# Kernel tuning notes

Measured on AMD Instinct MI355X. Metric: run time of the kernel, lower is better.

## Reference

```python
import jax, jax.numpy as jnp
import numpy as np

B, L, D, H, PD = 1, 512, 1024, 16, 128
HW = D // H  # 64


def _layernorm(x, g, b, eps=1e-5):
    mu = jnp.mean(x, axis=-1, keepdims=True)
    var = jnp.var(x, axis=-1, keepdims=True)
    return (x - mu) * jax.lax.rsqrt(var + eps) * g + b


def setup_inputs() -> dict:
    key = jax.random.key(0)
    ks = jax.random.split(key, 16)
    s = 0.02
    return {
        "sequence_state": jax.random.normal(ks[0], (B, L, D), jnp.float32),
        "pairwise_state": jax.random.normal(ks[1], (B, L, L, PD), jnp.float32),
        "mask": jnp.ones((B, L), dtype=bool),
        # layernorm before attention
        "ln1_g": jnp.ones((D,), jnp.float32),
        "ln1_b": jnp.zeros((D,), jnp.float32),
        # attention params (weights stored [in, out])
        "proj_w": jax.random.normal(ks[2], (D, 3 * H * HW), jnp.float32) * s,
        "g_w": jax.random.normal(ks[3], (D, H * HW), jnp.float32) * s,
        "g_b": jnp.ones((H * HW,), jnp.float32),
        "o_w": jax.random.normal(ks[4], (H * HW, D), jnp.float32) * s,
        "o_b": jnp.zeros((D,), jnp.float32),
        # pair-to-sequence bias
        "p2s_ln_g": jnp.ones((PD,), jnp.float32),
        "p2s_ln_b": jnp.zeros((PD,), jnp.float32),
        "p2s_w": jax.random.normal(ks[5], (PD, H), jnp.float32) * s,
        # residue MLP
        "mlp_ln_g": jnp.ones((D,), jnp.float32),
        "mlp_ln_b": jnp.zeros((D,), jnp.float32),
        "mlp_w1": jax.random.normal(ks[6], (D, 4 * D), jnp.float32) * s,
        "mlp_b1": jnp.zeros((4 * D,), jnp.float32),
        "mlp_w2": jax.random.normal(ks[7], (4 * D, D), jnp.float32) * s,
        "mlp_b2": jnp.zeros((D,), jnp.float32),
    }


def reference(sequence_state, pairwise_state, mask,
              ln1_g, ln1_b, proj_w, g_w, g_b, o_w, o_b,
              p2s_ln_g, p2s_ln_b, p2s_w,
              mlp_ln_g, mlp_ln_b, mlp_w1, mlp_b1, mlp_w2, mlp_b2):
    # PairToSequence: LN over pairwise feature dim, then project to per-head bias
    z = _layernorm(pairwise_state, p2s_ln_g, p2s_ln_b)
    bias = jnp.einsum("bqkp,ph->bhqk", z, p2s_w)  # [B,H,L,L]

    # Pre-attention layernorm
    y = _layernorm(sequence_state, ln1_g, ln1_b)

    # Gated attention with pairwise bias
    t = (y @ proj_w).reshape(B, L, H, 3 * HW)
    q, k, v = jnp.split(t, 3, axis=-1)  # each [B,L,H,HW]
    q = q * (HW ** -0.5)
    a = jnp.einsum("bqhc,bkhc->bhqk", q, k) + bias
    a = jnp.where(mask[:, None, None, :], a, -jnp.inf)
    a = jax.nn.softmax(a, axis=-1)
    o = jnp.einsum("bhqk,bkhc->bqhc", a, v).reshape(B, L, H * HW)
    gate = jax.nn.sigmoid(y @ g_w + g_b)
    o = (gate * o) @ o_w + o_b

    # residual (dropout=0 -> identity)
    s = sequence_state + o

    # ResidueMLP: x + Linear(ReLU(Linear(LN(x))))
    h = _layernorm(s, mlp_ln_g, mlp_ln_b)
    h = jax.nn.relu(h @ mlp_w1 + mlp_b1) @ mlp_w2 + mlp_b2
    return s + h
```

## Files before the change

### kernel.cpp

```cpp
#include <hip/hip_runtime.h>


typedef __attribute__((ext_vector_type(8))) short bfrag;
typedef __attribute__((ext_vector_type(4))) float f32x4;
typedef unsigned short ushort_t;
typedef unsigned int u32;

#define AS1 __attribute__((address_space(1)))
#define AS3 __attribute__((address_space(3)))

__device__ __forceinline__ void gll16(const void* g, void* l) {
  __builtin_amdgcn_global_load_lds((const AS1 u32*)g, (AS3 u32*)l, 16, 0, 0);
}

__device__ __forceinline__ unsigned short f2b(float x) {
  union { float f; unsigned u; } a; a.f = x;
  unsigned r = a.u + 0x7fffu + ((a.u >> 16) & 1u);
  return (unsigned short)(r >> 16);
}
__device__ __forceinline__ unsigned pack2(float a, float b) {
  return (unsigned)f2b(a) | ((unsigned)f2b(b) << 16);
}
__device__ __forceinline__ float b2f(ushort_t u) {
  union { float f; unsigned v; } a; a.v = ((unsigned)u) << 16; return a.f;
}

#define OFF_BIASH ((size_t)0)
#define OFF_Y     ((size_t)8388608)
#define OFF_QS    (OFF_Y    + (size_t)1048576)
#define OFF_KS    (OFF_QS   + (size_t)1048576)
#define OFF_VT    (OFF_KS   + (size_t)1048576)
#define OFF_GATE  (OFF_VT   + (size_t)1048576)
#define OFF_OG    (OFF_GATE + (size_t)2097152)
#define OFF_S     (OFF_OG   + (size_t)1048576)
#define OFF_HLN   (OFF_S    + (size_t)2097152)
#define OFF_H1    (OFF_HLN  + (size_t)1048576)
#define OFF_WPG   (OFF_H1   + (size_t)4194304)
#define OFF_WO    (OFF_WPG  + (size_t)8388608)
#define OFF_W1    (OFF_WO   + (size_t)2097152)
#define OFF_W2    (OFF_W1   + (size_t)8388608)

__device__ __forceinline__ void transp_tile(
    const float* __restrict__ W, ushort_t* __restrict__ Wt, int K, int N,
    int bx, int by, int tid, float* smem) {
  float (*tile)[65] = (float(*)[65])smem;
  int n0 = bx * 64, k0 = by * 64;
  int tr = tid >> 4, tc = (tid & 15) * 4;
#pragma unroll
  for (int i = 0; i < 4; i++) {
    int r = tr + i * 16;
    float4 v = *(const float4*)&W[(long)(k0 + r) * N + n0 + tc];
    tile[r][tc] = v.x; tile[r][tc + 1] = v.y; tile[r][tc + 2] = v.z; tile[r][tc + 3] = v.w;
  }
  __syncthreads();
  int nr = tid >> 2, kk = (tid & 3) * 16;
  ushort_t* dst = Wt + (long)(n0 + nr) * K + k0 + kk;
  uint4 q;
  q.x = pack2(tile[kk + 0][nr], tile[kk + 1][nr]);
  q.y = pack2(tile[kk + 2][nr], tile[kk + 3][nr]);
  q.z = pack2(tile[kk + 4][nr], tile[kk + 5][nr]);
  q.w = pack2(tile[kk + 6][nr], tile[kk + 7][nr]);
  *(uint4*)dst = q;
  uint4 q2;
  q2.x = pack2(tile[kk + 8][nr],  tile[kk + 9][nr]);
  q2.y = pack2(tile[kk + 10][nr], tile[kk + 11][nr]);
  q2.z = pack2(tile[kk + 12][nr], tile[kk + 13][nr]);
  q2.w = pack2(tile[kk + 14][nr], tile[kk + 15][nr]);
  *(uint4*)(dst + 8) = q2;
}

__global__ __launch_bounds__(256) void mega1(
    const float* __restrict__ pw,
    const float* __restrict__ p2s_g, const float* __restrict__ p2s_b,
    const float* __restrict__ p2s_w,
    const float* __restrict__ proj_w, const float* __restrict__ g_w,
    const float* __restrict__ o_w, const float* __restrict__ w1,
    const float* __restrict__ w2,
    const float* __restrict__ seq, const float* __restrict__ ln1_g,
    const float* __restrict__ ln1_b, const float* __restrict__ o_b,
    ushort_t* __restrict__ biasH, ushort_t* __restrict__ wpg,
    ushort_t* __restrict__ wo, ushort_t* __restrict__ w1t,
    ushort_t* __restrict__ w2t, ushort_t* __restrict__ ybf,
    float* __restrict__ sbuf) {
  __shared__ float smemF[5920];
  const int id = blockIdx.x, t = threadIdx.x;

  if (id < 4096) {
    ushort_t* wb  = (ushort_t*)smemF;
    ushort_t* zsb = wb + 2048;
    ushort_t* res = zsb + 64 * 136;
    const int w = t >> 6, lane = t & 63, ln = lane & 15, quad = lane >> 4;
    const long pair0 = (long)id * 64;
    const int p = t >> 2, j = t & 3;

#pragma unroll
    for (int i = t; i < 2048; i += 256) {
      int f = i >> 4, hh = i & 15;
      int chunk = f >> 5, q2 = (f >> 3) & 3, jj = f & 7;
      wb[(chunk * 64 + q2 * 16 + hh) * 8 + jj] = f2b(p2s_w[i]);
    }

    const float4* xsrc = (const float4*)(pw + (pair0 + p) * 128 + j * 32);
    float4 xv[8];
#pragma unroll
    for (int q = 0; q < 8; q++) xv[q] = xsrc[q];
    float s = 0.f, sq = 0.f;
#pragma unroll
    for (int q = 0; q < 8; q++) {
      s  += xv[q].x + xv[q].y + xv[q].z + xv[q].w;
      sq += xv[q].x*xv[q].x + xv[q].y*xv[q].y + xv[q].z*xv[q].z + xv[q].w*xv[q].w;
    }
    s  += __shfl_xor(s, 1);  s  += __shfl_xor(s, 2);
    sq += __shfl_xor(sq, 1); sq += __shfl_xor(sq, 2);
    float mu = s * (1.f / 128.f);
    float rs = rsqrtf(sq * (1.f / 128.f) - mu * mu + 1e-5f);

    const float4* g4 = (const float4*)(p2s_g + j * 32);
    const float4* b4 = (const float4*)(p2s_b + j * 32);
    uint4* zdst = (uint4*)&zsb[p * 136 + j * 32];
#pragma unroll
    for (int q = 0; q < 4; q++) {
      float4 x0 = xv[2*q], x1 = xv[2*q+1];
      float4 g0 = g4[2*q], g1 = g4[2*q+1];
      float4 b0 = b4[2*q], b1 = b4[2*q+1];
      uint4 o;
      o.x = pack2((x0.x-mu)*rs*g0.x + b0.x, (x0.y-mu)*rs*g0.y + b0.y);
      o.y = pack2((x0.z-mu)*rs*g0.z + b0.z, (x0.w-mu)*rs*g0.w + b0.w);
      o.z = pack2((x1.x-mu)*rs*g1.x + b1.x, (x1.y-mu)*rs*g1.y + b1.y);
      o.w = pack2((x1.z-mu)*rs*g1.z + b1.z, (x1.w-mu)*rs*g1.w + b1.w);
      zdst[q] = o;
    }
    __syncthreads();

    f32x4 acc = (f32x4){0.f, 0.f, 0.f, 0.f};
#pragma unroll
    for (int chunk = 0; chunk < 4; chunk++) {
      bfrag a  = *(const bfrag*)&zsb[(w * 16 + ln) * 136 + chunk * 32 + quad * 8];
      bfrag bf = *(const bfrag*)&wb[(chunk * 64 + quad * 16 + ln) * 8];
      acc = __builtin_amdgcn_mfma_f32_16x16x32_bf16(a, bf, acc, 0, 0, 0);
    }
    *(uint2*)&res[ln * 68 + w * 16 + quad * 4] =
        (uint2){pack2(acc[0], acc[1]), pack2(acc[2], acc[3])};
    __syncthreads();
    {
      int hh = t >> 4, base = (t & 15) * 4;
      *(uint2*)&biasH[(long)hh * 262144 + pair0 + base] =
          *(const uint2*)&res[hh * 68 + base];
    }
  } else if (id < 7424) {
    int j = id - 4096;
    if (j < 768)       transp_tile(proj_w, wpg, 1024, 3072, j % 48, j / 48, t, smemF);
    else if (j < 1024) { j -= 768;  transp_tile(g_w, wpg + (long)3072 * 1024, 1024, 1024, j % 16, j / 16, t, smemF); }
    else if (j < 1280) { j -= 1024; transp_tile(o_w, wo, 1024, 1024, j % 16, j / 16, t, smemF); }
    else if (j < 2304) { j -= 1280; transp_tile(w1, w1t, 1024, 4096, j % 64, j / 64, t, smemF); }
    else               { j -= 2304; transp_tile(w2, w2t, 4096, 1024, j % 16, j / 16, t, smemF); }
  } else {
    int row = id - 7424;
    long base = (long)row * 1024 + t * 4;
    float4 v = *(const float4*)(seq + base);
    float4 ob = *(const float4*)(o_b + t * 4);
    float4 sv; sv.x = v.x + ob.x; sv.y = v.y + ob.y; sv.z = v.z + ob.z; sv.w = v.w + ob.w;
    *(float4*)(sbuf + base) = sv;
    float s  = v.x + v.y + v.z + v.w;
    float sq = v.x*v.x + v.y*v.y + v.z*v.z + v.w*v.w;
#pragma unroll
    for (int k = 1; k < 64; k <<= 1) { s += __shfl_xor(s, k); sq += __shfl_xor(sq, k); }
    if ((t & 63) == 0) { smemF[t >> 6] = s; smemF[4 + (t >> 6)] = sq; }
    __syncthreads();
    s  = smemF[0] + smemF[1] + smemF[2] + smemF[3];
    sq = smemF[4] + smemF[5] + smemF[6] + smemF[7];
    float mu = s * (1.f / 1024.f);
    float rsd = rsqrtf(sq * (1.f / 1024.f) - mu * mu + 1e-5f);
    float4 gv = *(const float4*)(ln1_g + t * 4);
    float4 bv = *(const float4*)(ln1_b + t * 4);
    uint2 o;
    o.x = pack2((v.x - mu) * rsd * gv.x + bv.x, (v.y - mu) * rsd * gv.y + bv.y);
    o.y = pack2((v.z - mu) * rsd * gv.z + bv.z, (v.w - mu) * rsd * gv.w + bv.w);
    *(uint2*)(ybf + base) = o;
  }
}

template <int EPI>
__global__ __launch_bounds__(256) void gemm128(
    const ushort_t* __restrict__ A, const ushort_t* __restrict__ Bt,
    int lda, int ldb, int Ksplit,
    const float* __restrict__ bias1,
    float* __restrict__ outF, ushort_t* __restrict__ outH, int ldc,
    ushort_t* __restrict__ qs, ushort_t* __restrict__ ks,
    ushort_t* __restrict__ vt, float* __restrict__ gatebuf) {
  __shared__ ushort_t As[64 * 32];
  __shared__ ushort_t Bs[128 * 32];
  const int tid = threadIdx.x;
  const int w = tid >> 6, lane = tid & 63;
  const int ln = lane & 15, quad = lane >> 4;
  const int wm = w >> 1, wn = w & 1;
  const int m0 = blockIdx.y * 64, n0 = blockIdx.x * 128;
  const int z = blockIdx.z;
  const int Koff = (EPI == 7) ? z * Ksplit : 0;

  const ushort_t* ga  = A  + (long)(m0 + (tid >> 2)) * lda + Koff + (tid & 3) * 8;
  const ushort_t* gb0 = Bt + (long)(n0 + (tid >> 2)) * ldb + Koff + (tid & 3) * 8;
  const ushort_t* gb1 = gb0 + (long)64 * ldb;
  unsigned wofs = __builtin_amdgcn_readfirstlane(w * 1024);
  char* lA  = (char*)As + wofs;
  char* lB0 = (char*)Bs + wofs;
  char* lB1 = (char*)Bs + 4096 + wofs;

  f32x4 acc[2][4];
#pragma unroll
  for (int i = 0; i < 2; i++)
#pragma unroll
    for (int j = 0; j < 4; j++) acc[i][j] = (f32x4){0.f, 0.f, 0.f, 0.f};

  for (int k0 = 0; k0 < Ksplit; k0 += 32) {
    gll16(ga + k0, lA);
    gll16(gb0 + k0, lB0);
    gll16(gb1 + k0, lB1);
    __syncthreads();
    bfrag a0 = *(const bfrag*)&As[(wm * 32 + ln) * 32 + quad * 8];
    bfrag a1 = *(const bfrag*)&As[(wm * 32 + 16 + ln) * 32 + quad * 8];
#pragma unroll
    for (int bn = 0; bn < 4; bn++) {
      bfrag b = *(const bfrag*)&Bs[(wn * 64 + bn * 16 + ln) * 32 + quad * 8];
      acc[0][bn] = __builtin_amdgcn_mfma_f32_16x16x32_bf16(a0, b, acc[0][bn], 0, 0, 0);
      acc[1][bn] = __builtin_amdgcn_mfma_f32_16x16x32_bf16(a1, b, acc[1][bn], 0, 0, 0);
    }
    __syncthreads();
  }

#pragma unroll
  for (int am = 0; am < 2; am++) {
#pragma unroll
    for (int bn = 0; bn < 4; bn++) {
      int ocol = n0 + wn * 64 + bn * 16 + ln;
#pragma unroll
      for (int r = 0; r < 4; r++) {
        int orow = m0 + wm * 32 + am * 16 + quad * 4 + r;
        float v = acc[am][bn][r];
        if (EPI == 3) {
          v = fmaxf(v + bias1[ocol], 0.f);
          outH[(long)orow * ldc + ocol] = f2b(v);
        } else if (EPI == 6) {
          if (ocol < 3072) {
            int h = ocol / 192, j = ocol - h * 192;
            if (j < 64)       qs[((long)h * 512 + orow) * 64 + j] = f2b(v * 0.125f);
            else if (j < 128) ks[((long)h * 512 + orow) * 64 + (j - 64)] = f2b(v);
            else              vt[((long)h * 64 + (j - 128)) * 512 + orow] = f2b(v);
          } else {
            int gcol = ocol - 3072;
            float gv = v + bias1[gcol];
            gatebuf[(long)orow * 1024 + gcol] = 1.f / (1.f + __expf(-gv));
          }
        } else {
          atomicAdd(&outF[(long)orow * ldc + ocol], v);
        }
      }
    }
  }
}

__global__ __launch_bounds__(256) void flash_attn(
    const ushort_t* __restrict__ qs, const ushort_t* __restrict__ ks,
    const ushort_t* __restrict__ vt, const ushort_t* __restrict__ biasH,
    const float* __restrict__ gate, ushort_t* __restrict__ og) {
  __shared__ ushort_t Qs[32 * 72];
  __shared__ ushort_t Ks[64 * 72];
  __shared__ ushort_t Vs[64 * 72];
  __shared__ ushort_t Ps[32 * 72];
  __shared__ float redm[4][16];
  __shared__ float reds[4][16];
  const int tid = threadIdx.x;
  const int w = tid >> 6, lane = tid & 63, ln = lane & 15, quad = lane >> 4;
  const int wm = w >> 1, wn = w & 1;
  const int h = blockIdx.x, q0 = blockIdx.y * 32;

  {
    int r = tid >> 3, c0 = (tid & 7) * 8;
    *(uint4*)&Qs[r * 72 + c0] = *(const uint4*)(qs + ((long)(h * 512 + q0 + r)) * 64 + c0);
  }

  float m_[4], l_[4];
  f32x4 Oacc[2];
#pragma unroll
  for (int i = 0; i < 4; i++) { m_[i] = -1e30f; l_[i] = 0.f; }
  Oacc[0] = (f32x4){0.f,0.f,0.f,0.f};
  Oacc[1] = (f32x4){0.f,0.f,0.f,0.f};

  const int rkv = tid >> 2, ckv = (tid & 3) * 16;

  for (int kt = 0; kt < 8; kt++) {
    const int k0 = kt * 64;
    __syncthreads();
    { const ushort_t* srcK = ks + ((long)(h * 512 + k0 + rkv)) * 64 + ckv;
      *(uint4*)&Ks[rkv * 72 + ckv]     = *(const uint4*)srcK;
      *(uint4*)&Ks[rkv * 72 + ckv + 8] = *(const uint4*)(srcK + 8);
      const ushort_t* srcV = vt + ((long)(h * 64 + rkv)) * 512 + k0 + ckv;
      *(uint4*)&Vs[rkv * 72 + ckv]     = *(const uint4*)srcV;
      *(uint4*)&Vs[rkv * 72 + ckv + 8] = *(const uint4*)(srcV + 8); }

    f32x4 acc[2];
    const ushort_t* bp = biasH + ((long)h * 512 + q0 + wm * 16 + quad * 4) * 512
                         + k0 + wn * 32 + ln;
#pragma unroll
    for (int t4 = 0; t4 < 2; t4++)
#pragma unroll
      for (int rr = 0; rr < 4; rr++)
        acc[t4][rr] = b2f(bp[(long)rr * 512 + t4 * 16]);

    __syncthreads();
#pragma unroll
    for (int s = 0; s < 2; s++) {
      bfrag a = *(const bfrag*)&Qs[(wm * 16 + ln) * 72 + s * 32 + quad * 8];
#pragma unroll
      for (int t4 = 0; t4 < 2; t4++) {
        bfrag b = *(const bfrag*)&Ks[(wn * 32 + t4 * 16 + ln) * 72 + s * 32 + quad * 8];
        acc[t4] = __builtin_amdgcn_mfma_f32_16x16x32_bf16(a, b, acc[t4], 0, 0, 0);
      }
    }

    float mt[4];
#pragma unroll
    for (int rr = 0; rr < 4; rr++) mt[rr] = fmaxf(acc[0][rr], acc[1][rr]);
#pragma unroll
    for (int xm = 1; xm < 16; xm <<= 1)
#pragma unroll
      for (int rr = 0; rr < 4; rr++) mt[rr] = fmaxf(mt[rr], __shfl_xor(mt[rr], xm));
    if (ln == 0)
#pragma unroll
      for (int rr = 0; rr < 4; rr++) redm[w][quad * 4 + rr] = mt[rr];
    __syncthreads();
#pragma unroll
    for (int rr = 0; rr < 4; rr++) mt[rr] = fmaxf(mt[rr], redm[w ^ 1][quad * 4 + rr]);

    float al[4];
#pragma unroll
    for (int rr = 0; rr < 4; rr++) {
      float mn = fmaxf(m_[rr], mt[rr]);
      al[rr] = __expf(m_[rr] - mn);
      m_[rr] = mn;
    }
#pragma unroll
    for (int t4 = 0; t4 < 2; t4++)
#pragma unroll
      for (int rr = 0; rr < 4; rr++)
        acc[t4][rr] = __expf(acc[t4][rr] - m_[rr]);

    float rsl[4];
#pragma unroll
    for (int rr = 0; rr < 4; rr++) rsl[rr] = acc[0][rr] + acc[1][rr];
#pragma unroll
    for (int xm = 1; xm < 16; xm <<= 1)
#pragma unroll
      for (int rr = 0; rr < 4; rr++) rsl[rr] += __shfl_xor(rsl[rr], xm);
    if (ln == 0)
#pragma unroll
      for (int rr = 0; rr < 4; rr++) reds[w][quad * 4 + rr] = rsl[rr];

#pragma unroll
    for (int t4 = 0; t4 < 2; t4++)
#pragma unroll
      for (int rr = 0; rr < 4; rr++)
        Ps[(wm * 16 + quad * 4 + rr) * 72 + wn * 32 + t4 * 16 + ln] = f2b(acc[t4][rr]);
    __syncthreads();

#pragma unroll
    for (int rr = 0; rr < 4; rr++) {
      float rtot = rsl[rr] + reds[w ^ 1][quad * 4 + rr];
      l_[rr] = l_[rr] * al[rr] + rtot;
    }
#pragma unroll
    for (int t4 = 0; t4 < 2; t4++)
#pragma unroll
      for (int rr = 0; rr < 4; rr++) Oacc[t4][rr] *= al[rr];

#pragma unroll
    for (int s = 0; s < 2; s++) {
      bfrag a = *(const bfrag*)&Ps[(wm * 16 + ln) * 72 + s * 32 + quad * 8];
#pragma unroll
      for (int t4 = 0; t4 < 2; t4++) {
        bfrag b = *(const bfrag*)&Vs[(wn * 32 + t4 * 16 + ln) * 72 + s * 32 + quad * 8];
        Oacc[t4] = __builtin_amdgcn_mfma_f32_16x16x32_bf16(a, b, Oacc[t4], 0, 0, 0);
      }
    }
  }

#pragma unroll
  for (int t4 = 0; t4 < 2; t4++) {
#pragma unroll
    for (int rr = 0; rr < 4; rr++) {
      int grow = q0 + wm * 16 + quad * 4 + rr;
      int gcol = h * 64 + wn * 32 + t4 * 16 + ln;
      float gt = gate[(long)grow * 1024 + gcol];
      og[(long)grow * 1024 + gcol] = f2b(Oacc[t4][rr] / l_[rr] * gt);
    }
  }
}

__global__ __launch_bounds__(256) void ln2(
    const float* __restrict__ sbuf, const float* __restrict__ g,
    const float* __restrict__ b, const float* __restrict__ b2,
    ushort_t* __restrict__ hln, float* __restrict__ out) {
  __shared__ float ps[8];
  int row = blockIdx.x, t = threadIdx.x;
  long base = (long)row * 1024 + t * 4;
  float4 v = *(const float4*)(sbuf + base);
  float4 b2v = *(const float4*)(b2 + t * 4);
  float4 ov; ov.x = v.x + b2v.x; ov.y = v.y + b2v.y; ov.z = v.z + b2v.z; ov.w = v.w + b2v.w;
  *(float4*)(out + base) = ov;
  float s  = v.x + v.y + v.z + v.w;
  float sq = v.x*v.x + v.y*v.y + v.z*v.z + v.w*v.w;
#pragma unroll
  for (int k = 1; k < 64; k <<= 1) { s += __shfl_xor(s, k); sq += __shfl_xor(sq, k); }
  if ((t & 63) == 0) { ps[t >> 6] = s; ps[4 + (t >> 6)] = sq; }
  __syncthreads();
  s  = ps[0] + ps[1] + ps[2] + ps[3];
  sq = ps[4] + ps[5] + ps[6] + ps[7];
  float mu = s * (1.f / 1024.f);
  float rsd = rsqrtf(sq * (1.f / 1024.f) - mu * mu + 1e-5f);
  float4 gv = *(const float4*)(g + t * 4);
  float4 bv = *(const float4*)(b + t * 4);
  uint2 o;
  o.x = pack2((v.x - mu) * rsd * gv.x + bv.x, (v.y - mu) * rsd * gv.y + bv.y);
  o.y = pack2((v.z - mu) * rsd * gv.z + bv.z, (v.w - mu) * rsd * gv.w + bv.w);
  *(uint2*)(hln + base) = o;
}

extern "C" void kernel_launch(void* const* d_in, const int* in_sizes, int n_in,
                              void* d_out, int out_size, void* d_ws, size_t ws_size,
                              hipStream_t stream) {
  const float* seq    = (const float*)d_in[0];
  const float* pw     = (const float*)d_in[1];
  const float* ln1_g  = (const float*)d_in[3];
  const float* ln1_b  = (const float*)d_in[4];
  const float* proj_w = (const float*)d_in[5];
  const float* g_w    = (const float*)d_in[6];
  const float* g_b    = (const float*)d_in[7];
  const float* o_w    = (const float*)d_in[8];
  const float* o_b    = (const float*)d_in[9];
  const float* p2s_g  = (const float*)d_in[10];
  const float* p2s_b  = (const float*)d_in[11];
  const float* p2s_w  = (const float*)d_in[12];
  const float* mlp_g  = (const float*)d_in[13];
  const float* mlp_bb = (const float*)d_in[14];
  const float* w1     = (const float*)d_in[15];
  const float* b1     = (const float*)d_in[16];
  const float* w2     = (const float*)d_in[17];
  const float* b2     = (const float*)d_in[18];
  float* out = (float*)d_out;
  char* ws = (char*)d_ws;

  ushort_t* biasH = (ushort_t*)(ws + OFF_BIASH);
  ushort_t* ybf   = (ushort_t*)(ws + OFF_Y);
  ushort_t* qs    = (ushort_t*)(ws + OFF_QS);
  ushort_t* ks    = (ushort_t*)(ws + OFF_KS);
  ushort_t* vt    = (ushort_t*)(ws + OFF_VT);
  float* gatebuf  = (float*)(ws + OFF_GATE);
  ushort_t* og    = (ushort_t*)(ws + OFF_OG);
  float* sbuf     = (float*)(ws + OFF_S);
  ushort_t* hln   = (ushort_t*)(ws + OFF_HLN);
  ushort_t* h1    = (ushort_t*)(ws + OFF_H1);
  ushort_t* wpg   = (ushort_t*)(ws + OFF_WPG);
  ushort_t* wo    = (ushort_t*)(ws + OFF_WO);
  ushort_t* w1t   = (ushort_t*)(ws + OFF_W1);
  ushort_t* w2t   = (ushort_t*)(ws + OFF_W2);

  mega1<<<7936, 256, 0, stream>>>(pw, p2s_g, p2s_b, p2s_w,
                                  proj_w, g_w, o_w, w1, w2,
                                  seq, ln1_g, ln1_b, o_b,
                                  biasH, wpg, wo, w1t, w2t, ybf, sbuf);
  gemm128<6><<<dim3(32, 8, 1), 256, 0, stream>>>(ybf, wpg, 1024, 1024, 1024,
                                                 g_b, nullptr, nullptr, 0,
                                                 qs, ks, vt, gatebuf);
  flash_attn<<<dim3(16, 16), 256, 0, stream>>>(qs, ks, vt, biasH, gatebuf, og);
  gemm128<7><<<dim3(8, 8, 4), 256, 0, stream>>>(og, wo, 1024, 1024, 256,
                                                nullptr, sbuf, nullptr, 1024,
                                                nullptr, nullptr, nullptr, nullptr);
  ln2<<<512, 256, 0, stream>>>(sbuf, mlp_g, mlp_bb, b2, hln, out);
  gemm128<3><<<dim3(32, 8, 1), 256, 0, stream>>>(hln, w1t, 1024, 1024, 1024,
                                                 b1, nullptr, h1, 4096,
                                                 nullptr, nullptr, nullptr, nullptr);
  gemm128<7><<<dim3(8, 8, 4), 256, 0, stream>>>(h1, w2t, 4096, 4096, 1024,
                                                nullptr, out, nullptr, 1024,
                                                nullptr, nullptr, nullptr, nullptr);
}
```

Measured before the change: 368.7 us.

## Double-buffer 64x64 GEMMs, split flash-attn keys per wave, nontemporal pair loads

The GEMM shrinks from 64x128 to 64x64 tiles, doubling the grid, and double-buffers its LDS loads so the next K-slice is fetched while MFMAs run. Flash attention now has each wave own a half of the key columns with its own running max and sum, which removes the per-tile cross-wave reductions and barriers; the two halves are merged through LDS at the end. The pairwise LayerNorm loads switch to nontemporal, interleaved float4 accesses, and the weight transpose also uses nontemporal loads. Smaller tiles lower reuse per block, and the final merge adds extra LDS traffic and synchronisation.

Result: faster. 326.9 us (-11.3%).

```diff
diff --git a/kernel.cpp b/kernel.cpp
--- a/kernel.cpp
+++ b/kernel.cpp
@@ -49,7 +49,8 @@
 #pragma unroll
   for (int i = 0; i < 4; i++) {
     int r = tr + i * 16;
-    float4 v = *(const float4*)&W[(long)(k0 + r) * N + n0 + tc];
+    f32x4 v = __builtin_nontemporal_load(
+        (const f32x4*)&W[(long)(k0 + r) * N + n0 + tc]);
     tile[r][tc] = v.x; tile[r][tc + 1] = v.y; tile[r][tc + 2] = v.z; tile[r][tc + 3] = v.w;
   }
   __syncthreads();
@@ -91,7 +92,8 @@
     ushort_t* res = zsb + 64 * 136;
     const int w = t >> 6, lane = t & 63, ln = lane & 15, quad = lane >> 4;
     const long pair0 = (long)id * 64;
-    const int p = t >> 2, j = t & 3;
+    const int p = w * 16 + (lane >> 2);
+    const int j = lane & 3;
 
 #pragma unroll
     for (int i = t; i < 2048; i += 256) {
@@ -100,35 +102,30 @@
       wb[(chunk * 64 + q2 * 16 + hh) * 8 + jj] = f2b(p2s_w[i]);
     }
 
-    const float4* xsrc = (const float4*)(pw + (pair0 + p) * 128 + j * 32);
-    float4 xv[8];
-#pragma unroll
-    for (int q = 0; q < 8; q++) xv[q] = xsrc[q];
+    const float* xbase = pw + (pair0 + p) * 128 + j * 4;
+    f32x4 xv[8];
+#pragma unroll
+    for (int q = 0; q < 8; q++)
+      xv[q] = __builtin_nontemporal_load((const f32x4*)(xbase + q * 16));
     float s = 0.f, sq = 0.f;
 #pragma unroll
     for (int q = 0; q < 8; q++) {
       s  += xv[q].x + xv[q].y + xv[q].z + xv[q].w;
       sq += xv[q].x*xv[q].x + xv[q].y*xv[q].y + xv[q].z*xv[q].z + xv[q].w*xv[q].w;
     }
-    s  += __shfl_xor(s, 1);  s  += __shfl_xor(s, 2);
+    s += __shfl_xor(s, 1); s += __shfl_xor(s, 2);
     sq += __shfl_xor(sq, 1); sq += __shfl_xor(sq, 2);
     float mu = s * (1.f / 128.f);
     float rs = rsqrtf(sq * (1.f / 128.f) - mu * mu + 1e-5f);
 
-    const float4* g4 = (const float4*)(p2s_g + j * 32);
-    const float4* b4 = (const float4*)(p2s_b + j * 32);
-    uint4* zdst = (uint4*)&zsb[p * 136 + j * 32];
-#pragma unroll
-    for (int q = 0; q < 4; q++) {
-      float4 x0 = xv[2*q], x1 = xv[2*q+1];
-      float4 g0 = g4[2*q], g1 = g4[2*q+1];
-      float4 b0 = b4[2*q], b1 = b4[2*q+1];
-      uint4 o;
-      o.x = pack2((x0.x-mu)*rs*g0.x + b0.x, (x0.y-mu)*rs*g0.y + b0.y);
-      o.y = pack2((x0.z-mu)*rs*g0.z + b0.z, (x0.w-mu)*rs*g0.w + b0.w);
-      o.z = pack2((x1.x-mu)*rs*g1.x + b1.x, (x1.y-mu)*rs*g1.y + b1.y);
-      o.w = pack2((x1.z-mu)*rs*g1.z + b1.z, (x1.w-mu)*rs*g1.w + b1.w);
-      zdst[q] = o;
+#pragma unroll
+    for (int q = 0; q < 8; q++) {
+      f32x4 gv = *(const f32x4*)(p2s_g + j * 4 + q * 16);
+      f32x4 bv = *(const f32x4*)(p2s_b + j * 4 + q * 16);
+      uint2 o;
+      o.x = pack2((xv[q].x - mu) * rs * gv.x + bv.x, (xv[q].y - mu) * rs * gv.y + bv.y);
+      o.y = pack2((xv[q].z - mu) * rs * gv.z + bv.z, (xv[q].w - mu) * rs * gv.w + bv.w);
+      *(uint2*)&zsb[p * 136 + q * 16 + j * 4] = o;
     }
     __syncthreads();
 
@@ -181,58 +178,62 @@
 }
 
 template <int EPI>
-__global__ __launch_bounds__(256) void gemm128(
+__global__ __launch_bounds__(256) void gemm64(
     const ushort_t* __restrict__ A, const ushort_t* __restrict__ Bt,
     int lda, int ldb, int Ksplit,
     const float* __restrict__ bias1,
     float* __restrict__ outF, ushort_t* __restrict__ outH, int ldc,
     ushort_t* __restrict__ qs, ushort_t* __restrict__ ks,
     ushort_t* __restrict__ vt, float* __restrict__ gatebuf) {
-  __shared__ ushort_t As[64 * 32];
-  __shared__ ushort_t Bs[128 * 32];
+  __shared__ ushort_t As[2][64 * 32];
+  __shared__ ushort_t Bs[2][64 * 32];
   const int tid = threadIdx.x;
   const int w = tid >> 6, lane = tid & 63;
   const int ln = lane & 15, quad = lane >> 4;
   const int wm = w >> 1, wn = w & 1;
-  const int m0 = blockIdx.y * 64, n0 = blockIdx.x * 128;
+  const int m0 = blockIdx.y * 64, n0 = blockIdx.x * 64;
   const int z = blockIdx.z;
   const int Koff = (EPI == 7) ? z * Ksplit : 0;
 
-  const ushort_t* ga  = A  + (long)(m0 + (tid >> 2)) * lda + Koff + (tid & 3) * 8;
-  const ushort_t* gb0 = Bt + (long)(n0 + (tid >> 2)) * ldb + Koff + (tid & 3) * 8;
-  const ushort_t* gb1 = gb0 + (long)64 * ldb;
+  const ushort_t* ga = A  + (long)(m0 + (tid >> 2)) * lda + Koff + (tid & 3) * 8;
+  const ushort_t* gb = Bt + (long)(n0 + (tid >> 2)) * ldb + Koff + (tid & 3) * 8;
   unsigned wofs = __builtin_amdgcn_readfirstlane(w * 1024);
-  char* lA  = (char*)As + wofs;
-  char* lB0 = (char*)Bs + wofs;
-  char* lB1 = (char*)Bs + 4096 + wofs;
-
-  f32x4 acc[2][4];
+  char* lA[2] = {(char*)&As[0][0] + wofs, (char*)&As[1][0] + wofs};
+  char* lB[2] = {(char*)&Bs[0][0] + wofs, (char*)&Bs[1][0] + wofs};
+
+  f32x4 acc[2][2];
 #pragma unroll
   for (int i = 0; i < 2; i++)
 #pragma unroll
-    for (int j = 0; j < 4; j++) acc[i][j] = (f32x4){0.f, 0.f, 0.f, 0.f};
-
+    for (int jj = 0; jj < 2; jj++) acc[i][jj] = (f32x4){0.f, 0.f, 0.f, 0.f};
+
+  gll16(ga, lA[0]);
+  gll16(gb, lB[0]);
+  int buf = 0;
   for (int k0 = 0; k0 < Ksplit; k0 += 32) {
-    gll16(ga + k0, lA);
-    gll16(gb0 + k0, lB0);
-    gll16(gb1 + k0, lB1);
-    __syncthreads();
-    bfrag a0 = *(const bfrag*)&As[(wm * 32 + ln) * 32 + quad * 8];
-    bfrag a1 = *(const bfrag*)&As[(wm * 32 + 16 + ln) * 32 + quad * 8];
-#pragma unroll
-    for (int bn = 0; bn < 4; bn++) {
-      bfrag b = *(const bfrag*)&Bs[(wn * 64 + bn * 16 + ln) * 32 + quad * 8];
-      acc[0][bn] = __builtin_amdgcn_mfma_f32_16x16x32_bf16(a0, b, acc[0][bn], 0, 0, 0);
-      acc[1][bn] = __builtin_amdgcn_mfma_f32_16x16x32_bf16(a1, b, acc[1][bn], 0, 0, 0);
-    }
-    __syncthreads();
+    __syncthreads();
+    if (k0 + 32 < Ksplit) {
+      gll16(ga + k0 + 32, lA[buf ^ 1]);
+      gll16(gb + k0 + 32, lB[buf ^ 1]);
+    }
+    const ushort_t* Ab = &As[buf][0];
+    const ushort_t* Bb = &Bs[buf][0];
+    bfrag a0 = *(const bfrag*)&Ab[(wm * 32 + ln) * 32 + quad * 8];
+    bfrag a1 = *(const bfrag*)&Ab[(wm * 32 + 16 + ln) * 32 + quad * 8];
+    bfrag b0 = *(const bfrag*)&Bb[(wn * 32 + ln) * 32 + quad * 8];
+    bfrag b1 = *(const bfrag*)&Bb[(wn * 32 + 16 + ln) * 32 + quad * 8];
+    acc[0][0] = __builtin_amdgcn_mfma_f32_16x16x32_bf16(a0, b0, acc[0][0], 0, 0, 0);
+    acc[0][1] = __builtin_amdgcn_mfma_f32_16x16x32_bf16(a0, b1, acc[0][1], 0, 0, 0);
+    acc[1][0] = __builtin_amdgcn_mfma_f32_16x16x32_bf16(a1, b0, acc[1][0], 0, 0, 0);
+    acc[1][1] = __builtin_amdgcn_mfma_f32_16x16x32_bf16(a1, b1, acc[1][1], 0, 0, 0);
+    buf ^= 1;
   }
 
 #pragma unroll
   for (int am = 0; am < 2; am++) {
 #pragma unroll
-    for (int bn = 0; bn < 4; bn++) {
-      int ocol = n0 + wn * 64 + bn * 16 + ln;
+    for (int bn = 0; bn < 2; bn++) {
+      int ocol = n0 + wn * 32 + bn * 16 + ln;
 #pragma unroll
       for (int r = 0; r < 4; r++) {
         int orow = m0 + wm * 32 + am * 16 + quad * 4 + r;
@@ -242,10 +243,10 @@
           outH[(long)orow * ldc + ocol] = f2b(v);
         } else if (EPI == 6) {
           if (ocol < 3072) {
-            int h = ocol / 192, j = ocol - h * 192;
-            if (j < 64)       qs[((long)h * 512 + orow) * 64 + j] = f2b(v * 0.125f);
-            else if (j < 128) ks[((long)h * 512 + orow) * 64 + (j - 64)] = f2b(v);
-            else              vt[((long)h * 64 + (j - 128)) * 512 + orow] = f2b(v);
+            int h = ocol / 192, jq = ocol - h * 192;
+            if (jq < 64)       qs[((long)h * 512 + orow) * 64 + jq] = f2b(v * 0.125f);
+            else if (jq < 128) ks[((long)h * 512 + orow) * 64 + (jq - 64)] = f2b(v);
+            else               vt[((long)h * 64 + (jq - 128)) * 512 + orow] = f2b(v);
           } else {
             int gcol = ocol - 3072;
             float gv = v + bias1[gcol];
@@ -266,40 +267,34 @@
   __shared__ ushort_t Qs[32 * 72];
   __shared__ ushort_t Ks[64 * 72];
   __shared__ ushort_t Vs[64 * 72];
-  __shared__ ushort_t Ps[32 * 72];
-  __shared__ float redm[4][16];
-  __shared__ float reds[4][16];
+  __shared__ ushort_t Ps[4][16 * 40];
   const int tid = threadIdx.x;
   const int w = tid >> 6, lane = tid & 63, ln = lane & 15, quad = lane >> 4;
   const int wm = w >> 1, wn = w & 1;
   const int h = blockIdx.x, q0 = blockIdx.y * 32;
 
-  {
-    int r = tid >> 3, c0 = (tid & 7) * 8;
-    *(uint4*)&Qs[r * 72 + c0] = *(const uint4*)(qs + ((long)(h * 512 + q0 + r)) * 64 + c0);
-  }
+  { int r = tid >> 3, c = (tid & 7) * 8;
+    *(uint4*)&Qs[r * 72 + c] = *(const uint4*)(qs + ((long)(h * 512 + q0 + r)) * 64 + c); }
 
   float m_[4], l_[4];
-  f32x4 Oacc[2];
-#pragma unroll
-  for (int i = 0; i < 4; i++) { m_[i] = -1e30f; l_[i] = 0.f; }
-  Oacc[0] = (f32x4){0.f,0.f,0.f,0.f};
-  Oacc[1] = (f32x4){0.f,0.f,0.f,0.f};
+  f32x4 Oacc[4];
+#pragma unroll
+  for (int i = 0; i < 4; i++) { m_[i] = -1e30f; l_[i] = 0.f; Oacc[i] = (f32x4){0.f,0.f,0.f,0.f}; }
 
   const int rkv = tid >> 2, ckv = (tid & 3) * 16;
 
   for (int kt = 0; kt < 8; kt++) {
     const int k0 = kt * 64;
     __syncthreads();
-    { const ushort_t* srcK = ks + ((long)(h * 512 + k0 + rkv)) * 64 + ckv;
-      *(uint4*)&Ks[rkv * 72 + ckv]     = *(const uint4*)srcK;
-      *(uint4*)&Ks[rkv * 72 + ckv + 8] = *(const uint4*)(srcK + 8);
-      const ushort_t* srcV = vt + ((long)(h * 64 + rkv)) * 512 + k0 + ckv;
-      *(uint4*)&Vs[rkv * 72 + ckv]     = *(const uint4*)srcV;
-      *(uint4*)&Vs[rkv * 72 + ckv + 8] = *(const uint4*)(srcV + 8); }
+    { const ushort_t* sk = ks + ((long)(h * 512 + k0 + rkv)) * 64 + ckv;
+      *(uint4*)&Ks[rkv * 72 + ckv]     = *(const uint4*)sk;
+      *(uint4*)&Ks[rkv * 72 + ckv + 8] = *(const uint4*)(sk + 8);
+      const ushort_t* sv = vt + ((long)(h * 64 + rkv)) * 512 + k0 + ckv;
+      *(uint4*)&Vs[rkv * 72 + ckv]     = *(const uint4*)sv;
+      *(uint4*)&Vs[rkv * 72 + ckv + 8] = *(const uint4*)(sv + 8); }
 
     f32x4 acc[2];
-    const ushort_t* bp = biasH + ((long)h * 512 + q0 + wm * 16 + quad * 4) * 512
+    const ushort_t* bp = biasH + ((long)(h * 512 + q0 + wm * 16 + quad * 4)) * 512
                          + k0 + wn * 32 + ln;
 #pragma unroll
     for (int t4 = 0; t4 < 2; t4++)
@@ -325,13 +320,6 @@
     for (int xm = 1; xm < 16; xm <<= 1)
 #pragma unroll
       for (int rr = 0; rr < 4; rr++) mt[rr] = fmaxf(mt[rr], __shfl_xor(mt[rr], xm));
-    if (ln == 0)
-#pragma unroll
-      for (int rr = 0; rr < 4; rr++) redm[w][quad * 4 + rr] = mt[rr];
-    __syncthreads();
-#pragma unroll
-    for (int rr = 0; rr < 4; rr++) mt[rr] = fmaxf(mt[rr], redm[w ^ 1][quad * 4 + rr]);
-
     float al[4];
 #pragma unroll
     for (int rr = 0; rr < 4; rr++) {
@@ -344,7 +332,6 @@
 #pragma unroll
       for (int rr = 0; rr < 4; rr++)
         acc[t4][rr] = __expf(acc[t4][rr] - m_[rr]);
-
     float rsl[4];
 #pragma unroll
     for (int rr = 0; rr < 4; rr++) rsl[rr] = acc[0][rr] + acc[1][rr];
@@ -352,46 +339,72 @@
     for (int xm = 1; xm < 16; xm <<= 1)
 #pragma unroll
       for (int rr = 0; rr < 4; rr++) rsl[rr] += __shfl_xor(rsl[rr], xm);
-    if (ln == 0)
-#pragma unroll
-      for (int rr = 0; rr < 4; rr++) reds[w][quad * 4 + rr] = rsl[rr];
+#pragma unroll
+    for (int rr = 0; rr < 4; rr++) l_[rr] = l_[rr] * al[rr] + rsl[rr];
+#pragma unroll
+    for (int t4 = 0; t4 < 4; t4++)
+#pragma unroll
+      for (int rr = 0; rr < 4; rr++) Oacc[t4][rr] *= al[rr];
 
 #pragma unroll
     for (int t4 = 0; t4 < 2; t4++)
 #pragma unroll
       for (int rr = 0; rr < 4; rr++)
-        Ps[(wm * 16 + quad * 4 + rr) * 72 + wn * 32 + t4 * 16 + ln] = f2b(acc[t4][rr]);
-    __syncthreads();
-
-#pragma unroll
-    for (int rr = 0; rr < 4; rr++) {
-      float rtot = rsl[rr] + reds[w ^ 1][quad * 4 + rr];
-      l_[rr] = l_[rr] * al[rr] + rtot;
-    }
-#pragma unroll
-    for (int t4 = 0; t4 < 2; t4++)
-#pragma unroll
-      for (int rr = 0; rr < 4; rr++) Oacc[t4][rr] *= al[rr];
-
-#pragma unroll
-    for (int s = 0; s < 2; s++) {
-      bfrag a = *(const bfrag*)&Ps[(wm * 16 + ln) * 72 + s * 32 + quad * 8];
-#pragma unroll
-      for (int t4 = 0; t4 < 2; t4++) {
-        bfrag b = *(const bfrag*)&Vs[(wn * 32 + t4 * 16 + ln) * 72 + s * 32 + quad * 8];
+        Ps[w][(quad * 4 + rr) * 40 + t4 * 16 + ln] = f2b(acc[t4][rr]);
+    __builtin_amdgcn_wave_barrier();
+    __builtin_amdgcn_s_waitcnt(0xC07F);
+    __builtin_amdgcn_wave_barrier();
+
+    {
+      bfrag a = *(const bfrag*)&Ps[w][ln * 40 + quad * 8];
+#pragma unroll
+      for (int t4 = 0; t4 < 4; t4++) {
+        bfrag b = *(const bfrag*)&Vs[(t4 * 16 + ln) * 72 + wn * 32 + quad * 8];
         Oacc[t4] = __builtin_amdgcn_mfma_f32_16x16x32_bf16(a, b, Oacc[t4], 0, 0, 0);
       }
     }
   }
 
-#pragma unroll
-  for (int t4 = 0; t4 < 2; t4++) {
+  __syncthreads();
+  float* ml = (float*)(void*)Ks;
+  if (ln == 0)
 #pragma unroll
     for (int rr = 0; rr < 4; rr++) {
-      int grow = q0 + wm * 16 + quad * 4 + rr;
-      int gcol = h * 64 + wn * 32 + t4 * 16 + ln;
-      float gt = gate[(long)grow * 1024 + gcol];
-      og[(long)grow * 1024 + gcol] = f2b(Oacc[t4][rr] / l_[rr] * gt);
+      ml[(w * 16 + quad * 4 + rr) * 2 + 0] = m_[rr];
+      ml[(w * 16 + quad * 4 + rr) * 2 + 1] = l_[rr];
+    }
+  __syncthreads();
+  const int pw_ = wm * 2 + (wn ^ 1);
+  float a_self[4];
+#pragma unroll
+  for (int rr = 0; rr < 4; rr++) {
+    float mo = ml[(pw_ * 16 + quad * 4 + rr) * 2 + 0];
+    float lo = ml[(pw_ * 16 + quad * 4 + rr) * 2 + 1];
+    float mF = fmaxf(m_[rr], mo);
+    a_self[rr] = __expf(m_[rr] - mF);
+    l_[rr] = l_[rr] * a_self[rr] + lo * __expf(mo - mF);
+  }
+  float* Of = (float*)(void*)Vs;
+  if (wn == 1) {
+#pragma unroll
+    for (int t4 = 0; t4 < 4; t4++)
+#pragma unroll
+      for (int rr = 0; rr < 4; rr++)
+        Of[(wm * 16 + quad * 4 + rr) * 68 + t4 * 16 + ln] = Oacc[t4][rr] * a_self[rr];
+  }
+  __syncthreads();
+  if (wn == 0) {
+#pragma unroll
+    for (int t4 = 0; t4 < 4; t4++) {
+#pragma unroll
+      for (int rr = 0; rr < 4; rr++) {
+        int grow = q0 + wm * 16 + quad * 4 + rr;
+        int gcol = h * 64 + t4 * 16 + ln;
+        float v = Oacc[t4][rr] * a_self[rr]
+                + Of[(wm * 16 + quad * 4 + rr) * 68 + t4 * 16 + ln];
+        v /= l_[rr];
+        og[(long)grow * 1024 + gcol] = f2b(v * gate[(long)grow * 1024 + gcol]);
+      }
     }
   }
 }
@@ -468,18 +481,18 @@
                                   proj_w, g_w, o_w, w1, w2,
                                   seq, ln1_g, ln1_b, o_b,
                                   biasH, wpg, wo, w1t, w2t, ybf, sbuf);
-  gemm128<6><<<dim3(32, 8, 1), 256, 0, stream>>>(ybf, wpg, 1024, 1024, 1024,
-                                                 g_b, nullptr, nullptr, 0,
-                                                 qs, ks, vt, gatebuf);
+  gemm64<6><<<dim3(64, 8, 1), 256, 0, stream>>>(ybf, wpg, 1024, 1024, 1024,
+                                                g_b, nullptr, nullptr, 0,
+                                                qs, ks, vt, gatebuf);
   flash_attn<<<dim3(16, 16), 256, 0, stream>>>(qs, ks, vt, biasH, gatebuf, og);
-  gemm128<7><<<dim3(8, 8, 4), 256, 0, stream>>>(og, wo, 1024, 1024, 256,
+  gemm64<7><<<dim3(16, 8, 4), 256, 0, stream>>>(og, wo, 1024, 1024, 256,
                                                 nullptr, sbuf, nullptr, 1024,
                                                 nullptr, nullptr, nullptr, nullptr);
   ln2<<<512, 256, 0, stream>>>(sbuf, mlp_g, mlp_bb, b2, hln, out);
-  gemm128<3><<<dim3(32, 8, 1), 256, 0, stream>>>(hln, w1t, 1024, 1024, 1024,
-                                                 b1, nullptr, h1, 4096,
-                                                 nullptr, nullptr, nullptr, nullptr);
-  gemm128<7><<<dim3(8, 8, 4), 256, 0, stream>>>(h1, w2t, 4096, 4096, 1024,
+  gemm64<3><<<dim3(64, 8, 1), 256, 0, stream>>>(hln, w1t, 1024, 1024, 1024,
+                                                b1, nullptr, h1, 4096,
+                                                nullptr, nullptr, nullptr, nullptr);
+  gemm64<7><<<dim3(16, 8, 4), 256, 0, stream>>>(h1, w2t, 4096, 4096, 1024,
                                                 nullptr, out, nullptr, 1024,
                                                 nullptr, nullptr, nullptr, nullptr);
 }
```
